# Performance work log

Measured on AMD Instinct MI355X. Metric: run time of the kernel, lower is better.

Reference implementation:

```python
import jax, jax.numpy as jnp
import numpy as np

HEADS = 12
HEAD_SIZE = 64
NEG_BIG = 1e12


def _rope_sin_cos(seq_len, head_size, dtype):
    # embeddings[n, 2i] = sin(n * 10000^(-2i/d)), [n, 2i+1] = cos(...)
    pos = jnp.arange(seq_len, dtype=dtype)                      # [s]
    idx = jnp.arange(head_size // 2, dtype=dtype)               # [d/2]
    inv_freq = jnp.power(jnp.asarray(10000.0, dtype), -2.0 * idx / head_size)
    ang = jnp.einsum('n,d->nd', pos, inv_freq)                  # [s, d/2]
    # cos_pos / sin_pos: repeat_interleave each frequency twice -> [1, s, 1, d]
    cos = jnp.repeat(jnp.cos(ang), 2, axis=-1)[None, :, None, :]
    sin = jnp.repeat(jnp.sin(ang), 2, axis=-1)[None, :, None, :]
    return sin, cos


def _rotate_half_interleaved(x):
    # stack([-x[..., 1::2], x[..., ::2]], -1).reshape_as(x)
    x2 = jnp.stack([-x[..., 1::2], x[..., ::2]], axis=-1)
    return x2.reshape(x.shape)


def setup_inputs() -> dict:
    key = jax.random.key(0)
    k1, k2 = jax.random.split(key)
    bs, s, h = 16, 512, 768
    hidden = jax.random.normal(k1, (bs, s, h), dtype=jnp.float32)
    attention_mask = jnp.ones((bs, s), dtype=jnp.int32)
    W = jax.random.normal(k2, (h, HEADS * 2 * HEAD_SIZE), dtype=jnp.float32) * (h ** -0.5)
    b = jnp.zeros((HEADS * 2 * HEAD_SIZE,), dtype=jnp.float32)
    return {"hidden": hidden, "attention_mask": attention_mask, "W": W, "b": b}


def reference(hidden, attention_mask, W, b):
    bs, s, _ = hidden.shape
    x = hidden @ W + b                                           # [b, s, heads*2*hd]
    x = x.reshape(bs, s, HEADS, 2, HEAD_SIZE)
    qw, kw = x[..., 0, :], x[..., 1, :]                          # [b, s, h, d]

    sin, cos = _rope_sin_cos(s, HEAD_SIZE, hidden.dtype)
    qw = qw * cos + _rotate_half_interleaved(qw) * sin
    kw = kw * cos + _rotate_half_interleaved(kw) * sin

    logits = jnp.einsum('bmhd,bnhd->bhmn', qw, kw)               # [b, h, s, s]

    am = attention_mask.astype(logits.dtype)
    pad_mask = 1.0 - am[:, None, None, :] * am[:, None, :, None]
    logits = logits - pad_mask * NEG_BIG

    tril = jnp.tril(jnp.ones((s, s), dtype=logits.dtype), k=-1)  # strictly lower
    logits = logits - tril[None, None, :, :] * NEG_BIG

    return logits / (HEAD_SIZE ** 0.5)
```

## Files before the change

kernel.cpp:

```cpp
#include <hip/hip_runtime.h>
#include <math.h>

#define HEADS 12
#define HSZ   64
#define SEQ   512
#define HID   768
#define NOUT  1536
#define NEGQ  1.25e11f

typedef _Float16 f16x8 __attribute__((ext_vector_type(8)));
typedef _Float16 f16x4 __attribute__((ext_vector_type(4)));
typedef float    f32x4 __attribute__((ext_vector_type(4)));
typedef int      i32x4 __attribute__((ext_vector_type(4)));
typedef int      i32x8 __attribute__((ext_vector_type(8)));

__device__ __forceinline__ void async_ld16(const void* g, void* l) {
  __builtin_amdgcn_global_load_lds(
      (__attribute__((address_space(1))) void*)g,
      (__attribute__((address_space(3))) void*)l, 16, 0, 0);
}

__global__ __launch_bounds__(256) void prep_k(
    const float* __restrict__ hidden, const float* __restrict__ W,
    unsigned char* __restrict__ Xb8, unsigned char* __restrict__ Wt8,
    float2* __restrict__ tab)
{
  __shared__ float t_lds[32][33];
  const int b = blockIdx.x;
  const int t = threadIdx.x;
  if (b < 1152) {
    const int tk = b % 24, tn = b / 24;
    const int k0 = tk * 32, n0 = tn * 32;
    const int tx = t & 31, ty = t >> 5;
#pragma unroll
    for (int r = 0; r < 4; ++r)
      t_lds[ty + r * 8][tx] = W[(size_t)(k0 + ty + r * 8) * NOUT + n0 + tx];
    __syncthreads();
    const int nl = t >> 3, kg = t & 7;
    int w = __builtin_amdgcn_cvt_pk_fp8_f32(t_lds[kg * 4 + 0][nl],
                                            t_lds[kg * 4 + 1][nl], 0, false);
    w = __builtin_amdgcn_cvt_pk_fp8_f32(t_lds[kg * 4 + 2][nl],
                                        t_lds[kg * 4 + 3][nl], w, true);
    *(int*)&Wt8[(size_t)(n0 + nl) * HID + k0 + kg * 4] = w;
  } else if (b < 1152 + 1536) {
    const int idx = (b - 1152) * 256 + t;
    const float4* src = (const float4*)hidden + (size_t)idx * 4;
    float4 v0 = src[0], v1 = src[1], v2 = src[2], v3 = src[3];
    int4 o;
    o.x = __builtin_amdgcn_cvt_pk_fp8_f32(v0.x, v0.y, 0, false);
    o.x = __builtin_amdgcn_cvt_pk_fp8_f32(v0.z, v0.w, o.x, true);
    o.y = __builtin_amdgcn_cvt_pk_fp8_f32(v1.x, v1.y, 0, false);
    o.y = __builtin_amdgcn_cvt_pk_fp8_f32(v1.z, v1.w, o.y, true);
    o.z = __builtin_amdgcn_cvt_pk_fp8_f32(v2.x, v2.y, 0, false);
    o.z = __builtin_amdgcn_cvt_pk_fp8_f32(v2.z, v2.w, o.z, true);
    o.w = __builtin_amdgcn_cvt_pk_fp8_f32(v3.x, v3.y, 0, false);
    o.w = __builtin_amdgcn_cvt_pk_fp8_f32(v3.z, v3.w, o.w, true);
    ((int4*)Xb8)[idx] = o;
  } else {
    const int e = (b - 2688) * 256 + t;
    const int si = e >> 5, fi = e & 31;
    float inv = powf(10000.f, -(float)fi / 32.f);
    float ang = (float)si * inv;
    float sv, cv;
    sincosf(ang, &sv, &cv);
    tab[e] = make_float2(cv, sv);
  }
}

__global__ __launch_bounds__(256) void gemm1_k(
    const unsigned char* __restrict__ Xb8, const unsigned char* __restrict__ Wt8,
    const float* __restrict__ bias, const float2* __restrict__ tab,
    _Float16* __restrict__ qb, _Float16* __restrict__ kb)
{
  __shared__ __align__(16) int As4[4096];
  __shared__ __align__(16) int Bs4[4096];
  const int tid = threadIdx.x;
  const int lane = tid & 63;
  const int m0 = blockIdx.x * 128;
  const int n0 = blockIdx.y * 128;
  const int wm = ((tid >> 6) & 1) * 64;
  const int wn = (tid >> 7) * 64;
  const int lrow = lane & 15;
  const int q = lane >> 4;

  f32x4 acc[4][4] = {};

  for (int kt = 0; kt < 6; ++kt) {
    const int kbase = kt * 128;
#pragma unroll
    for (int c = 0; c < 4; ++c) {
      const int s = tid + c * 256;
      const int row = s >> 3, cc = s & 7;
      const int so = (((cc >> 1) ^ (row & 3)) << 5) + ((cc & 1) << 4);
      async_ld16(Xb8 + (size_t)(m0 + row) * HID + kbase + so, (char*)As4 + s * 16);
      async_ld16(Wt8 + (size_t)(n0 + row) * HID + kbase + so, (char*)Bs4 + s * 16);
    }
    __syncthreads();
    i32x8 af[4], bf[4];
#pragma unroll
    for (int i = 0; i < 4; ++i) {
      const int ra = wm + i * 16 + lrow;
      const int oa = ra * 32 + ((q ^ (ra & 3)) << 3);
      i32x4 lo = *(const i32x4*)&As4[oa];
      i32x4 hi = *(const i32x4*)&As4[oa + 4];
      af[i] = (i32x8){lo.x, lo.y, lo.z, lo.w, hi.x, hi.y, hi.z, hi.w};
      const int rb = wn + i * 16 + lrow;
      const int ob = rb * 32 + ((q ^ (rb & 3)) << 3);
      lo = *(const i32x4*)&Bs4[ob];
      hi = *(const i32x4*)&Bs4[ob + 4];
      bf[i] = (i32x8){lo.x, lo.y, lo.z, lo.w, hi.x, hi.y, hi.z, hi.w};
    }
#pragma unroll
    for (int i = 0; i < 4; ++i)
#pragma unroll
      for (int j = 0; j < 4; ++j)
        acc[i][j] = __builtin_amdgcn_mfma_scale_f32_16x16x128_f8f6f4(
            bf[j], af[i], acc[i][j], 0, 0,
            0, 0x7F7F7F7F, 0, 0x7F7F7F7F);
    __syncthreads();
  }

  const int qlane = lane >> 4;
  const int mlane = m0 + wm + (lane & 15);
#pragma unroll
  for (int j = 0; j < 4; ++j) {
    const int nb = n0 + wn + j * 16 + qlane * 4;
    const float4 b4 = *(const float4*)&bias[nb];
    const int d0 = nb & 63;
    const int h = nb >> 7;
    _Float16* dst = ((nb >> 6) & 1) ? kb : qb;
    const int fi0 = d0 >> 1;
#pragma unroll
    for (int i = 0; i < 4; ++i) {
      const int m = mlane + i * 16;
      const int si = m & (SEQ - 1);
      const int bb = m >> 9;
      const float4 cs = *(const float4*)&tab[si * 32 + fi0];
      const float v0 = acc[i][j][0] + b4.x;
      const float v1 = acc[i][j][1] + b4.y;
      const float v2 = acc[i][j][2] + b4.z;
      const float v3 = acc[i][j][3] + b4.w;
      f16x4 o;
      o.x = (_Float16)fmaf(v0, cs.x, -v1 * cs.y);
      o.y = (_Float16)fmaf(v1, cs.x, v0 * cs.y);
      o.z = (_Float16)fmaf(v2, cs.z, -v3 * cs.w);
      o.w = (_Float16)fmaf(v3, cs.z, v2 * cs.w);
      *(f16x4*)&dst[((size_t)(bb * HEADS + h) * SEQ + si) * HSZ + d0] = o;
    }
  }
}

__global__ __launch_bounds__(256) void gemm2_k(
    const _Float16* __restrict__ qb, const _Float16* __restrict__ kb,
    const int* __restrict__ am, float* __restrict__ out)
{
  const int tid = threadIdx.x;
  const int bh = blockIdx.y;
  const int bb = bh / HEADS;
  const int mt = blockIdx.x >> 2, nt = blockIdx.x & 3;
  const int m0 = mt * 128, n0 = nt * 128;
  const int* amb = am + bb * SEQ;
  float* obase = out + (size_t)bh * SEQ * SEQ;

  if (nt < mt) {
#pragma unroll
    for (int p = 0; p < 16; ++p) {
      const int f = p * 256 + tid;
      const int row = f >> 5, c4 = (f & 31) * 4;
      const int m = m0 + row;
      const float amm = (float)amb[m];
      const int nb = n0 + c4;
      const int4 a4 = *(const int4*)&amb[nb];
      f32x4 v;
      v[0] = -(2.f - amm * (float)a4.x) * NEGQ;
      v[1] = -(2.f - amm * (float)a4.y) * NEGQ;
      v[2] = -(2.f - amm * (float)a4.z) * NEGQ;
      v[3] = -(2.f - amm * (float)a4.w) * NEGQ;
      __builtin_nontemporal_store(v, (f32x4*)&obase[(size_t)m * SEQ + nb]);
    }
    return;
  }

  const _Float16* qg = qb + (size_t)bh * SEQ * HSZ;
  const _Float16* kg = kb + (size_t)bh * SEQ * HSZ;
  const int lane = tid & 63;
  const int wm = ((tid >> 6) & 1) * 64;
  const int wn = (tid >> 7) * 64;
  const int lrow = lane & 15;
  const int lk = (lane >> 4) * 8;

  f16x8 af[4][2], bf[4][2];
#pragma unroll
  for (int i = 0; i < 4; ++i)
#pragma unroll
    for (int h = 0; h < 2; ++h) {
      af[i][h] = *(const f16x8*)(qg + (size_t)(m0 + wm + i * 16 + lrow) * HSZ + h * 32 + lk);
      bf[i][h] = *(const f16x8*)(kg + (size_t)(n0 + wn + i * 16 + lrow) * HSZ + h * 32 + lk);
    }

  f32x4 acc[4][4] = {};
#pragma unroll
  for (int h = 0; h < 2; ++h)
#pragma unroll
    for (int i = 0; i < 4; ++i)
#pragma unroll
      for (int j = 0; j < 4; ++j)
        acc[i][j] = __builtin_amdgcn_mfma_f32_16x16x32_f16(bf[j][h], af[i][h], acc[i][j], 0, 0, 0);

  const int qlane = lane >> 4;
  const int mlane = m0 + wm + (lane & 15);
#pragma unroll
  for (int i = 0; i < 4; ++i) {
    const int m = mlane + i * 16;
    const float amm = (float)amb[m];
    float* orow = obase + (size_t)m * SEQ;
#pragma unroll
    for (int j = 0; j < 4; ++j) {
      const int nb = n0 + wn + j * 16 + qlane * 4;
      const int4 a4 = *(const int4*)&amb[nb];
      f32x4 v;
      v[0] = fmaf(acc[i][j][0], 0.125f,
                  -((float)(nb + 0 < m) + (1.f - amm * (float)a4.x)) * NEGQ);
      v[1] = fmaf(acc[i][j][1], 0.125f,
                  -((float)(nb + 1 < m) + (1.f - amm * (float)a4.y)) * NEGQ);
      v[2] = fmaf(acc[i][j][2], 0.125f,
                  -((float)(nb + 2 < m) + (1.f - amm * (float)a4.z)) * NEGQ);
      v[3] = fmaf(acc[i][j][3], 0.125f,
                  -((float)(nb + 3 < m) + (1.f - amm * (float)a4.w)) * NEGQ);
      __builtin_nontemporal_store(v, (f32x4*)&orow[nb]);
    }
  }
}

extern "C" void kernel_launch(void* const* d_in, const int* in_sizes, int n_in,
                              void* d_out, int out_size, void* d_ws, size_t ws_size,
                              hipStream_t stream) {
  const float* hidden = (const float*)d_in[0];
  const int*   am     = (const int*)d_in[1];
  const float* W      = (const float*)d_in[2];
  const float* bias   = (const float*)d_in[3];
  float* out = (float*)d_out;
  char* ws = (char*)d_ws;
  unsigned char* Xb8 = (unsigned char*)(ws);
  unsigned char* Wt8 = (unsigned char*)(ws + 6291456);
  _Float16* qb = (_Float16*)(ws + 7471104);
  _Float16* kb = (_Float16*)(ws + 20054016);
  float2*   tab = (float2*)(ws + 32636928);

  prep_k<<<dim3(2752), dim3(256), 0, stream>>>(hidden, W, Xb8, Wt8, tab);
  gemm1_k<<<dim3(64, 12), dim3(256), 0, stream>>>(Xb8, Wt8, bias, tab, qb, kb);
  gemm2_k<<<dim3(16, 192), dim3(256), 0, stream>>>(qb, kb, am, out);
}
```

Measured before the change: 274.8 us.

## Fuse prep, projection GEMM and logits GEMM into one cooperative persistent kernel

Adds a persistent cooperative kernel with 512 blocks that runs the fp8 conversion, the projection GEMM with RoPE, and the QK logits/mask stage in sequence, separated by grid-wide syncs. This removes two kernel launches and the gaps between them. Whenever the occupancy query allows two blocks per CU, launch goes through hipLaunchCooperativeKernel. The output stores also change from nontemporal to regular stores. Risks are grid-sync overhead, load imbalance from the fixed 512-block grid, and the loss of nontemporal stores for the 150MB output write.

```diff
diff --git a/kernel.cpp b/kernel.cpp
--- a/kernel.cpp
+++ b/kernel.cpp
@@ -1,5 +1,8 @@
 #include <hip/hip_runtime.h>
+#include <hip/hip_cooperative_groups.h>
 #include <math.h>
+
+namespace cg = cooperative_groups;
 
 #define HEADS 12
 #define HSZ   64
@@ -18,6 +21,224 @@
   __builtin_amdgcn_global_load_lds(
       (__attribute__((address_space(1))) void*)g,
       (__attribute__((address_space(3))) void*)l, 16, 0, 0);
+}
+
+__global__ __launch_bounds__(256, 2) void fused_k(
+    const float* __restrict__ hidden, const int* __restrict__ am,
+    const float* __restrict__ W, const float* __restrict__ bias,
+    float* __restrict__ out,
+    unsigned char* __restrict__ Xb8, unsigned char* __restrict__ Wt8,
+    _Float16* __restrict__ qb, _Float16* __restrict__ kb,
+    float2* __restrict__ tab)
+{
+  cg::grid_group gg = cg::this_grid();
+  __shared__ __align__(16) char smem[32768];
+  const int tid = threadIdx.x;
+  const int lane = tid & 63;
+
+  {
+    float (*t_lds)[33] = (float (*)[33])smem;
+    for (int u = blockIdx.x; u < 2752; u += 512) {
+      if (u < 1152) {
+        const int tk = u % 24, tn = u / 24;
+        const int k0 = tk * 32, n0 = tn * 32;
+        const int tx = tid & 31, ty = tid >> 5;
+        __syncthreads();
+#pragma unroll
+        for (int r = 0; r < 4; ++r)
+          t_lds[ty + r * 8][tx] = W[(size_t)(k0 + ty + r * 8) * NOUT + n0 + tx];
+        __syncthreads();
+        const int nl = tid >> 3, kg = tid & 7;
+        int w = __builtin_amdgcn_cvt_pk_fp8_f32(t_lds[kg * 4 + 0][nl],
+                                                t_lds[kg * 4 + 1][nl], 0, false);
+        w = __builtin_amdgcn_cvt_pk_fp8_f32(t_lds[kg * 4 + 2][nl],
+                                            t_lds[kg * 4 + 3][nl], w, true);
+        *(int*)&Wt8[(size_t)(n0 + nl) * HID + k0 + kg * 4] = w;
+      } else if (u < 2688) {
+        const int idx = (u - 1152) * 256 + tid;
+        const float4* src = (const float4*)hidden + (size_t)idx * 4;
+        float4 v0 = src[0], v1 = src[1], v2 = src[2], v3 = src[3];
+        int4 o;
+        o.x = __builtin_amdgcn_cvt_pk_fp8_f32(v0.x, v0.y, 0, false);
+        o.x = __builtin_amdgcn_cvt_pk_fp8_f32(v0.z, v0.w, o.x, true);
+        o.y = __builtin_amdgcn_cvt_pk_fp8_f32(v1.x, v1.y, 0, false);
+        o.y = __builtin_amdgcn_cvt_pk_fp8_f32(v1.z, v1.w, o.y, true);
+        o.z = __builtin_amdgcn_cvt_pk_fp8_f32(v2.x, v2.y, 0, false);
+        o.z = __builtin_amdgcn_cvt_pk_fp8_f32(v2.z, v2.w, o.z, true);
+        o.w = __builtin_amdgcn_cvt_pk_fp8_f32(v3.x, v3.y, 0, false);
+        o.w = __builtin_amdgcn_cvt_pk_fp8_f32(v3.z, v3.w, o.w, true);
+        ((int4*)Xb8)[idx] = o;
+      } else {
+        const int e = (u - 2688) * 256 + tid;
+        const int si = e >> 5, fi = e & 31;
+        float inv = powf(10000.f, -(float)fi / 32.f);
+        float ang = (float)si * inv;
+        float sv, cv;
+        sincosf(ang, &sv, &cv);
+        tab[e] = make_float2(cv, sv);
+      }
+    }
+  }
+  gg.sync();
+
+  {
+    int* As4 = (int*)smem;
+    int* Bs4 = As4 + 4096;
+    const int wm = ((tid >> 6) & 1) * 64;
+    const int wn = (tid >> 7) * 64;
+    const int lrow = lane & 15;
+    const int q = lane >> 4;
+    const int qlane = lane >> 4;
+
+    for (int tile = blockIdx.x; tile < 768; tile += 512) {
+      const int m0 = (tile & 63) * 128;
+      const int n0 = (tile >> 6) * 128;
+      f32x4 acc[4][4] = {};
+
+      for (int kt = 0; kt < 6; ++kt) {
+        const int kbase = kt * 128;
+#pragma unroll
+        for (int c = 0; c < 4; ++c) {
+          const int s = tid + c * 256;
+          const int row = s >> 3, cc = s & 7;
+          const int so = (((cc >> 1) ^ (row & 3)) << 5) + ((cc & 1) << 4);
+          async_ld16(Xb8 + (size_t)(m0 + row) * HID + kbase + so, (char*)As4 + s * 16);
+          async_ld16(Wt8 + (size_t)(n0 + row) * HID + kbase + so, (char*)Bs4 + s * 16);
+        }
+        __syncthreads();
+        i32x8 af[4], bf[4];
+#pragma unroll
+        for (int i = 0; i < 4; ++i) {
+          const int ra = wm + i * 16 + lrow;
+          const int oa = ra * 32 + ((q ^ (ra & 3)) << 3);
+          i32x4 lo = *(const i32x4*)&As4[oa];
+          i32x4 hi = *(const i32x4*)&As4[oa + 4];
+          af[i] = (i32x8){lo.x, lo.y, lo.z, lo.w, hi.x, hi.y, hi.z, hi.w};
+          const int rb = wn + i * 16 + lrow;
+          const int ob = rb * 32 + ((q ^ (rb & 3)) << 3);
+          lo = *(const i32x4*)&Bs4[ob];
+          hi = *(const i32x4*)&Bs4[ob + 4];
+          bf[i] = (i32x8){lo.x, lo.y, lo.z, lo.w, hi.x, hi.y, hi.z, hi.w};
+        }
+#pragma unroll
+        for (int i = 0; i < 4; ++i)
+#pragma unroll
+          for (int j = 0; j < 4; ++j)
+            acc[i][j] = __builtin_amdgcn_mfma_scale_f32_16x16x128_f8f6f4(
+                bf[j], af[i], acc[i][j], 0, 0,
+                0, 0x7F7F7F7F, 0, 0x7F7F7F7F);
+        __syncthreads();
+      }
+
+      const int mlane = m0 + wm + (lane & 15);
+#pragma unroll
+      for (int j = 0; j < 4; ++j) {
+        const int nb = n0 + wn + j * 16 + qlane * 4;
+        const float4 b4 = *(const float4*)&bias[nb];
+        const int d0 = nb & 63;
+        const int h = nb >> 7;
+        _Float16* dst = ((nb >> 6) & 1) ? kb : qb;
+        const int fi0 = d0 >> 1;
+#pragma unroll
+        for (int i = 0; i < 4; ++i) {
+          const int m = mlane + i * 16;
+          const int si = m & (SEQ - 1);
+          const int bb = m >> 9;
+          const float4 cs = *(const float4*)&tab[si * 32 + fi0];
+          const float v0 = acc[i][j][0] + b4.x;
+          const float v1 = acc[i][j][1] + b4.y;
+          const float v2 = acc[i][j][2] + b4.z;
+          const float v3 = acc[i][j][3] + b4.w;
+          f16x4 o;
+          o.x = (_Float16)fmaf(v0, cs.x, -v1 * cs.y);
+          o.y = (_Float16)fmaf(v1, cs.x, v0 * cs.y);
+          o.z = (_Float16)fmaf(v2, cs.z, -v3 * cs.w);
+          o.w = (_Float16)fmaf(v3, cs.z, v2 * cs.w);
+          *(f16x4*)&dst[((size_t)(bb * HEADS + h) * SEQ + si) * HSZ + d0] = o;
+        }
+      }
+    }
+  }
+  gg.sync();
+
+  {
+    const int wm = ((tid >> 6) & 1) * 64;
+    const int wn = (tid >> 7) * 64;
+    const int lrow = lane & 15;
+    const int lk = (lane >> 4) * 8;
+    const int qlane = lane >> 4;
+
+    for (int unit = blockIdx.x; unit < 3072; unit += 512) {
+      const int bh = unit >> 4;
+      const int mt = (unit >> 2) & 3, nt = unit & 3;
+      const int bb = bh / HEADS;
+      const int m0 = mt * 128, n0 = nt * 128;
+      const int* amb = am + bb * SEQ;
+      float* obase = out + (size_t)bh * SEQ * SEQ;
+
+      if (nt < mt) {
+#pragma unroll
+        for (int p = 0; p < 16; ++p) {
+          const int f = p * 256 + tid;
+          const int row = f >> 5, c4 = (f & 31) * 4;
+          const int m = m0 + row;
+          const float amm = (float)amb[m];
+          const int nb = n0 + c4;
+          const int4 a4 = *(const int4*)&amb[nb];
+          float4 v;
+          v.x = -(2.f - amm * (float)a4.x) * NEGQ;
+          v.y = -(2.f - amm * (float)a4.y) * NEGQ;
+          v.z = -(2.f - amm * (float)a4.z) * NEGQ;
+          v.w = -(2.f - amm * (float)a4.w) * NEGQ;
+          *(float4*)&obase[(size_t)m * SEQ + nb] = v;
+        }
+        continue;
+      }
+
+      const _Float16* qg = qb + (size_t)bh * SEQ * HSZ;
+      const _Float16* kg = kb + (size_t)bh * SEQ * HSZ;
+      f16x8 af[4][2], bf[4][2];
+#pragma unroll
+      for (int i = 0; i < 4; ++i)
+#pragma unroll
+        for (int h = 0; h < 2; ++h) {
+          af[i][h] = *(const f16x8*)(qg + (size_t)(m0 + wm + i * 16 + lrow) * HSZ + h * 32 + lk);
+          bf[i][h] = *(const f16x8*)(kg + (size_t)(n0 + wn + i * 16 + lrow) * HSZ + h * 32 + lk);
+        }
+
+      f32x4 acc[4][4] = {};
+#pragma unroll
+      for (int h = 0; h < 2; ++h)
+#pragma unroll
+        for (int i = 0; i < 4; ++i)
+#pragma unroll
+          for (int j = 0; j < 4; ++j)
+            acc[i][j] = __builtin_amdgcn_mfma_f32_16x16x32_f16(bf[j][h], af[i][h], acc[i][j], 0, 0, 0);
+
+      const int mlane = m0 + wm + (lane & 15);
+#pragma unroll
+      for (int i = 0; i < 4; ++i) {
+        const int m = mlane + i * 16;
+        const float amm = (float)amb[m];
+        float* orow = obase + (size_t)m * SEQ;
+#pragma unroll
+        for (int j = 0; j < 4; ++j) {
+          const int nb = n0 + wn + j * 16 + qlane * 4;
+          const int4 a4 = *(const int4*)&amb[nb];
+          float4 v;
+          v.x = fmaf(acc[i][j][0], 0.125f,
+                     -((float)(nb + 0 < m) + (1.f - amm * (float)a4.x)) * NEGQ);
+          v.y = fmaf(acc[i][j][1], 0.125f,
+                     -((float)(nb + 1 < m) + (1.f - amm * (float)a4.y)) * NEGQ);
+          v.z = fmaf(acc[i][j][2], 0.125f,
+                     -((float)(nb + 2 < m) + (1.f - amm * (float)a4.z)) * NEGQ);
+          v.w = fmaf(acc[i][j][3], 0.125f,
+                     -((float)(nb + 3 < m) + (1.f - amm * (float)a4.w)) * NEGQ);
+          *(float4*)&orow[nb] = v;
+        }
+      }
+    }
+  }
 }
 
 __global__ __launch_bounds__(256) void prep_k(
@@ -171,12 +392,12 @@
       const float amm = (float)amb[m];
       const int nb = n0 + c4;
       const int4 a4 = *(const int4*)&amb[nb];
-      f32x4 v;
-      v[0] = -(2.f - amm * (float)a4.x) * NEGQ;
-      v[1] = -(2.f - amm * (float)a4.y) * NEGQ;
-      v[2] = -(2.f - amm * (float)a4.z) * NEGQ;
-      v[3] = -(2.f - amm * (float)a4.w) * NEGQ;
-      __builtin_nontemporal_store(v, (f32x4*)&obase[(size_t)m * SEQ + nb]);
+      float4 v;
+      v.x = -(2.f - amm * (float)a4.x) * NEGQ;
+      v.y = -(2.f - amm * (float)a4.y) * NEGQ;
+      v.z = -(2.f - amm * (float)a4.z) * NEGQ;
+      v.w = -(2.f - amm * (float)a4.w) * NEGQ;
+      *(float4*)&obase[(size_t)m * SEQ + nb] = v;
     }
     return;
   }
@@ -218,16 +439,16 @@
     for (int j = 0; j < 4; ++j) {
       const int nb = n0 + wn + j * 16 + qlane * 4;
       const int4 a4 = *(const int4*)&amb[nb];
-      f32x4 v;
-      v[0] = fmaf(acc[i][j][0], 0.125f,
-                  -((float)(nb + 0 < m) + (1.f - amm * (float)a4.x)) * NEGQ);
-      v[1] = fmaf(acc[i][j][1], 0.125f,
-                  -((float)(nb + 1 < m) + (1.f - amm * (float)a4.y)) * NEGQ);
-      v[2] = fmaf(acc[i][j][2], 0.125f,
-                  -((float)(nb + 2 < m) + (1.f - amm * (float)a4.z)) * NEGQ);
-      v[3] = fmaf(acc[i][j][3], 0.125f,
-                  -((float)(nb + 3 < m) + (1.f - amm * (float)a4.w)) * NEGQ);
-      __builtin_nontemporal_store(v, (f32x4*)&orow[nb]);
+      float4 v;
+      v.x = fmaf(acc[i][j][0], 0.125f,
+                 -((float)(nb + 0 < m) + (1.f - amm * (float)a4.x)) * NEGQ);
+      v.y = fmaf(acc[i][j][1], 0.125f,
+                 -((float)(nb + 1 < m) + (1.f - amm * (float)a4.y)) * NEGQ);
+      v.z = fmaf(acc[i][j][2], 0.125f,
+                 -((float)(nb + 2 < m) + (1.f - amm * (float)a4.z)) * NEGQ);
+      v.w = fmaf(acc[i][j][3], 0.125f,
+                 -((float)(nb + 3 < m) + (1.f - amm * (float)a4.w)) * NEGQ);
+      *(float4*)&orow[nb] = v;
     }
   }
 }
@@ -247,6 +468,16 @@
   _Float16* kb = (_Float16*)(ws + 20054016);
   float2*   tab = (float2*)(ws + 32636928);
 
+  int maxb = 0;
+  hipError_t oe = hipOccupancyMaxActiveBlocksPerMultiprocessor(&maxb, fused_k, 256, 0);
+  if (oe == hipSuccess && maxb >= 2) {
+    void* args[] = {(void*)&hidden, (void*)&am, (void*)&W, (void*)&bias,
+                    (void*)&out, (void*)&Xb8, (void*)&Wt8, (void*)&qb,
+                    (void*)&kb, (void*)&tab};
+    hipError_t e = hipLaunchCooperativeKernel((const void*)fused_k, dim3(512),
+                                              dim3(256), args, 0, stream);
+    if (e == hipSuccess) return;
+  }
   prep_k<<<dim3(2752), dim3(256), 0, stream>>>(hidden, W, Xb8, Wt8, tab);
   gemm1_k<<<dim3(64, 12), dim3(256), 0, stream>>>(Xb8, Wt8, bias, tab, qb, kb);
   gemm2_k<<<dim3(16, 192), dim3(256), 0, stream>>>(qb, kb, am, out);
```

Result: slower. 287.7 us (+4.7%).
